# Kernel tuning notes

Hardware: AMD Instinct MI355X
Metric: run time of the kernel (lower is better)

## Reference

```python
import jax, jax.numpy as jnp
import numpy as np

T, B, I, H = 512, 256, 256, 256


def setup_inputs() -> dict:
    key = jax.random.key(0)
    ks = jax.random.split(key, 4)
    s = 1.0 / np.sqrt(I + H)  # fan-in scaling like nn.Linear default
    return {
        "x": jax.random.normal(ks[0], (T, B, I), dtype=jnp.float32),
        "h": jnp.zeros((B, H), dtype=jnp.float32),
        "Wz_w": jax.random.normal(ks[1], (H, I + H), dtype=jnp.float32) * s,
        "Wz_b": jnp.zeros((H,), dtype=jnp.float32),
        "Wr_w": jax.random.normal(ks[2], (H, I + H), dtype=jnp.float32) * s,
        "Wr_b": jnp.zeros((H,), dtype=jnp.float32),
        "W_w": jax.random.normal(ks[3], (H, I + H), dtype=jnp.float32) * s,
        "W_b": jnp.zeros((H,), dtype=jnp.float32),
    }


def reference(x, h, Wz_w, Wz_b, Wr_w, Wr_b, W_w, W_b):
    # x: [T, B, I], h: [B, H]. Gate input order is cat(h, x) as in the torch code.
    def step(h, xt):
        gate = jnp.concatenate([h, xt], axis=1)              # [B, H+I]
        zt = jax.nn.sigmoid(gate @ Wz_w.T + Wz_b)            # [B, H]
        rt = jax.nn.sigmoid(gate @ Wr_w.T + Wr_b)            # [B, H]
        cand_in = jnp.concatenate([rt * h, xt], axis=1)      # [B, H+I]
        ht = (1.0 - zt) * h + zt * jnp.tanh(cand_in @ W_w.T + W_b)
        return ht, ht

    h_final, hAll = jax.lax.scan(step, h, x)                 # hAll: [T, B, H]
    return hAll, h_final
```

## Files before the change

### kernel.cpp

```cpp
#include <hip/hip_runtime.h>


typedef float f32x4 __attribute__((ext_vector_type(4)));
typedef short bf16x8 __attribute__((ext_vector_type(8)));

__device__ __forceinline__ unsigned short f2bf(float f) {
  union { float f; unsigned int u; } v; v.f = f;
  unsigned int u = v.u + 0x7fffu + ((v.u >> 16) & 1u);
  return (unsigned short)(u >> 16);
}
__device__ __forceinline__ float u2f(unsigned int u) {
  union { unsigned int u; float f; } v; v.u = u; return v.f;
}
__device__ __forceinline__ unsigned int cvt_pk_bf16(float lo, float hi) {
  unsigned int r;
  asm("v_cvt_pk_bf16_f32 %0, %1, %2" : "=v"(r) : "v"(lo), "v"(hi));
  return r;
}
__device__ __forceinline__ float sigmoid_f(float x) {
  return __builtin_amdgcn_rcpf(1.f + __expf(-x));
}
__device__ __forceinline__ float tanh_f(float x) {
  float e = __expf(2.f * x);
  return 1.f - 2.f * __builtin_amdgcn_rcpf(e + 1.f);
}
__device__ __forceinline__ f32x4 unpk(uint2 gv) {
  f32x4 a;
  a[0] = u2f(gv.x << 16); a[1] = u2f(gv.x & 0xffff0000u);
  a[2] = u2f(gv.y << 16); a[3] = u2f(gv.y & 0xffff0000u);
  return a;
}
__device__ __forceinline__ int frag_off(int j, int b) {
  return ((j >> 5) * 64 + ((j >> 3) & 3) * 16 + b) * 8 + (j & 7);
}

__global__ __launch_bounds__(256) void gru_gx_kernel(
    const float* __restrict__ x,
    const float* __restrict__ Wz, const float* __restrict__ Wr, const float* __restrict__ Wc,
    const float* __restrict__ bz, const float* __restrict__ br, const float* __restrict__ bc,
    unsigned short* __restrict__ gx)
{
  __shared__ __align__(16) unsigned short As[64][72];
  __shared__ __align__(16) unsigned short Bs[256][72];

  const int tid  = threadIdx.x;
  const int lane = tid & 63;
  const int wid  = tid >> 6;
  const int l15  = lane & 15;
  const int lg   = lane >> 4;
  const int m0   = blockIdx.x * 64;
  const int gate = blockIdx.y;
  const float* W    = (gate == 0) ? Wz : ((gate == 1) ? Wr : Wc);
  const float* bias = (gate == 0) ? bz : ((gate == 1) ? br : bc);

  f32x4 acc[16];
  #pragma unroll
  for (int n = 0; n < 16; ++n) acc[n] = (f32x4){0.f, 0.f, 0.f, 0.f};

  for (int k0 = 0; k0 < 256; k0 += 64) {
    #pragma unroll
    for (int i = 0; i < 4; ++i) {
      int idx = tid + i * 256;
      int row = idx >> 4;
      int kq  = (idx & 15) << 2;
      float4 v = *(const float4*)(x + (size_t)(m0 + row) * 256 + k0 + kq);
      uint2 p; p.x = cvt_pk_bf16(v.x, v.y); p.y = cvt_pk_bf16(v.z, v.w);
      *(uint2*)&As[row][kq] = p;
    }
    #pragma unroll
    for (int i = 0; i < 16; ++i) {
      int idx = tid + i * 256;
      int row = idx >> 4;
      int kq  = (idx & 15) << 2;
      float4 v = *(const float4*)(W + (size_t)row * 512 + 256 + k0 + kq);
      uint2 p; p.x = cvt_pk_bf16(v.x, v.y); p.y = cvt_pk_bf16(v.z, v.w);
      *(uint2*)&Bs[row][kq] = p;
    }
    __syncthreads();
    #pragma unroll
    for (int ks = 0; ks < 64; ks += 32) {
      bf16x8 af = *(const bf16x8*)&As[wid * 16 + l15][ks + lg * 8];
      #pragma unroll
      for (int n = 0; n < 16; ++n) {
        bf16x8 bf = *(const bf16x8*)&Bs[n * 16 + l15][ks + lg * 8];
        acc[n] = __builtin_amdgcn_mfma_f32_16x16x32_bf16(af, bf, acc[n], 0, 0, 0);
      }
    }
    __syncthreads();
  }

  unsigned short* Ts = &Bs[0][0];
  const int TS = 268;
  #pragma unroll
  for (int n = 0; n < 16; ++n) {
    const int j = n * 16 + l15;
    float bv = bias[j];
    #pragma unroll
    for (int r = 0; r < 4; ++r) {
      unsigned int pk = cvt_pk_bf16(acc[n][r] + bv, 0.f);
      Ts[(wid * 16 + lg * 4 + r) * TS + j] = (unsigned short)pk;
    }
  }
  __syncthreads();

  const int tt  = m0 >> 8;
  const int bg0 = (m0 & 255) >> 4;
  #pragma unroll
  for (int i = 0; i < 8; ++i) {
    int idx  = tid + i * 256;
    int bg_l = idx >> 9;
    int rem  = idx & 511;
    int cb_l = rem >> 3;
    int bp   = rem & 7;
    int m    = bg_l * 16 + bp * 2;
    uint2 lo = *(const uint2*)&Ts[(size_t)m * TS + cb_l * 4];
    uint2 hi = *(const uint2*)&Ts[(size_t)(m + 1) * TS + cb_l * 4];
    uint4 val; val.x = lo.x; val.y = lo.y; val.z = hi.x; val.w = hi.y;
    size_t off = (((size_t)tt * 16 + bg0 + bg_l) * 192 + gate * 64 + cb_l) * 64
                 + (size_t)bp * 8;
    *(uint4*)(gx + off) = val;
  }
}

__global__ __launch_bounds__(512, 1) void gru_rec_kernel(
    const unsigned short* __restrict__ gx,
    const float* __restrict__ h0,
    const float* __restrict__ Wz, const float* __restrict__ Wr, const float* __restrict__ Wc,
    float* __restrict__ out)
{
  __shared__ __align__(16) unsigned short hA[4096];
  __shared__ __align__(16) unsigned short rhA[4096];

  const int tid   = threadIdx.x;
  const int lane  = tid & 63;
  const int wid   = tid >> 6;
  const int l15   = lane & 15;
  const int lg    = lane >> 4;
  const int wg    = blockIdx.x;
  const int brow0 = wg * 16;
  const int cb    = wid * 32;

  bf16x8 wz[2][8], wr[2][8], wc[2][8];
  #pragma unroll
  for (int n = 0; n < 2; ++n) {
    const int j = cb + n * 16 + l15;
    #pragma unroll
    for (int kk = 0; kk < 8; ++kk) {
      const int k = kk * 32 + lg * 8;
      #pragma unroll
      for (int g = 0; g < 3; ++g) {
        const float* W = (g == 0) ? Wz : ((g == 1) ? Wr : Wc);
        const float* p = W + (size_t)j * 512 + k;
        float4 a = *(const float4*)p;
        float4 b = *(const float4*)(p + 4);
        bf16x8 f;
        f[0] = (short)f2bf(a.x); f[1] = (short)f2bf(a.y);
        f[2] = (short)f2bf(a.z); f[3] = (short)f2bf(a.w);
        f[4] = (short)f2bf(b.x); f[5] = (short)f2bf(b.y);
        f[6] = (short)f2bf(b.z); f[7] = (short)f2bf(b.w);
        if (g == 0) wz[n][kk] = f; else if (g == 1) wr[n][kk] = f; else wc[n][kk] = f;
      }
    }
  }

  f32x4 hreg[2];
  #pragma unroll
  for (int n = 0; n < 2; ++n)
    hreg[n] = *(const f32x4*)(h0 + (size_t)(brow0 + l15) * 256 + cb + n * 16 + lg * 4);
  for (int idx = tid; idx < 16 * 256; idx += 512) {
    int r = idx >> 8, c = idx & 255;
    hA[frag_off(c, r)] = f2bf(h0[(size_t)(brow0 + r) * 256 + c]);
  }

  uint2 g1z[2], g1r[2], g2[2];
  {
    const size_t tb = (size_t)wg * 12288;
    #pragma unroll
    for (int n = 0; n < 2; ++n) {
      g1z[n] = *(const uint2*)(gx + tb + (size_t)(wid * 8 + n * 4 + lg) * 64 + l15 * 4);
      g1r[n] = *(const uint2*)(gx + tb + (size_t)(64 + wid * 8 + n * 4 + lg) * 64 + l15 * 4);
      g2[n]  = *(const uint2*)(gx + tb + (size_t)(128 + wid * 8 + n * 4 + lg) * 64 + l15 * 4);
    }
  }
  __syncthreads();

  for (int t = 0; t < 512; ++t) {
    const int tn = (t < 511) ? (t + 1) : 511;
    const size_t tbn = ((size_t)tn * 16 + wg) * 12288;

    f32x4 accZ[2], accR[2];
    #pragma unroll
    for (int n = 0; n < 2; ++n) { accZ[n] = unpk(g1z[n]); accR[n] = unpk(g1r[n]); }
    #pragma unroll
    for (int n = 0; n < 2; ++n) {
      g1z[n] = *(const uint2*)(gx + tbn + (size_t)(wid * 8 + n * 4 + lg) * 64 + l15 * 4);
      g1r[n] = *(const uint2*)(gx + tbn + (size_t)(64 + wid * 8 + n * 4 + lg) * 64 + l15 * 4);
    }

    #pragma unroll
    for (int kk = 0; kk < 8; ++kk) {
      bf16x8 hf = *(const bf16x8*)&hA[kk * 512 + lane * 8];
      accZ[0] = __builtin_amdgcn_mfma_f32_16x16x32_bf16(wz[0][kk], hf, accZ[0], 0, 0, 0);
      accZ[1] = __builtin_amdgcn_mfma_f32_16x16x32_bf16(wz[1][kk], hf, accZ[1], 0, 0, 0);
      accR[0] = __builtin_amdgcn_mfma_f32_16x16x32_bf16(wr[0][kk], hf, accR[0], 0, 0, 0);
      accR[1] = __builtin_amdgcn_mfma_f32_16x16x32_bf16(wr[1][kk], hf, accR[1], 0, 0, 0);
    }
    f32x4 zreg[2];
    #pragma unroll
    for (int n = 0; n < 2; ++n) {
      #pragma unroll
      for (int r = 0; r < 4; ++r) zreg[n][r] = sigmoid_f(accZ[n][r]);
      float rh0 = sigmoid_f(accR[n][0]) * hreg[n][0];
      float rh1 = sigmoid_f(accR[n][1]) * hreg[n][1];
      float rh2 = sigmoid_f(accR[n][2]) * hreg[n][2];
      float rh3 = sigmoid_f(accR[n][3]) * hreg[n][3];
      uint2 pk; pk.x = cvt_pk_bf16(rh0, rh1); pk.y = cvt_pk_bf16(rh2, rh3);
      *(uint2*)&rhA[frag_off(cb + n * 16 + lg * 4, l15)] = pk;
    }
    asm volatile("s_waitcnt lgkmcnt(0)" ::: "memory");
    __builtin_amdgcn_s_barrier();
    __builtin_amdgcn_sched_barrier(0);

    f32x4 acc2[2];
    #pragma unroll
    for (int n = 0; n < 2; ++n) acc2[n] = unpk(g2[n]);
    #pragma unroll
    for (int n = 0; n < 2; ++n)
      g2[n] = *(const uint2*)(gx + tbn + (size_t)(128 + wid * 8 + n * 4 + lg) * 64 + l15 * 4);

    #pragma unroll
    for (int kk = 0; kk < 8; ++kk) {
      bf16x8 rf = *(const bf16x8*)&rhA[kk * 512 + lane * 8];
      acc2[0] = __builtin_amdgcn_mfma_f32_16x16x32_bf16(wc[0][kk], rf, acc2[0], 0, 0, 0);
      acc2[1] = __builtin_amdgcn_mfma_f32_16x16x32_bf16(wc[1][kk], rf, acc2[1], 0, 0, 0);
    }
    #pragma unroll
    for (int n = 0; n < 2; ++n) {
      #pragma unroll
      for (int r = 0; r < 4; ++r) {
        float th = tanh_f(acc2[n][r]);
        hreg[n][r] = hreg[n][r] + zreg[n][r] * (th - hreg[n][r]);
      }
      *(f32x4*)(out + (size_t)t * 65536 + (size_t)(brow0 + l15) * 256 + cb + n * 16 + lg * 4) = hreg[n];
      if (t == 511)
        *(f32x4*)(out + (size_t)33554432 + (size_t)(brow0 + l15) * 256 + cb + n * 16 + lg * 4) = hreg[n];
      uint2 pk; pk.x = cvt_pk_bf16(hreg[n][0], hreg[n][1]);
      pk.y = cvt_pk_bf16(hreg[n][2], hreg[n][3]);
      *(uint2*)&hA[frag_off(cb + n * 16 + lg * 4, l15)] = pk;
    }
    asm volatile("s_waitcnt lgkmcnt(0)" ::: "memory");
    __builtin_amdgcn_s_barrier();
    __builtin_amdgcn_sched_barrier(0);
  }
}

extern "C" void kernel_launch(void* const* d_in, const int* in_sizes, int n_in,
                              void* d_out, int out_size, void* d_ws, size_t ws_size,
                              hipStream_t stream) {
  const float* x  = (const float*)d_in[0];
  const float* h0 = (const float*)d_in[1];
  const float* Wz = (const float*)d_in[2];
  const float* bz = (const float*)d_in[3];
  const float* Wr = (const float*)d_in[4];
  const float* br = (const float*)d_in[5];
  const float* Wc = (const float*)d_in[6];
  const float* bc = (const float*)d_in[7];
  float* out = (float*)d_out;
  unsigned short* gxbuf = (unsigned short*)d_ws;

  dim3 gridA(2048, 3);
  gru_gx_kernel<<<gridA, 256, 0, stream>>>(x, Wz, Wr, Wc, bz, br, bc, gxbuf);
  gru_rec_kernel<<<16, 512, 0, stream>>>(gxbuf, h0, Wz, Wr, Wc, out);
}
```

Before: 1.042 ms.

## Fuse input-projection GEMM and recurrence into one kernel with per-timestep flags

Merges the gate-input GEMM and the sequential recurrence into one launch. The first 16 blocks run the recurrence, and the remaining blocks compute the gx tiles, each bumping a per-timestep atomic counter when its tile is written. Recurrence blocks spin on these counters so they can start before all of gx exists, overlapping the bulk GEMM with the serial loop. The risks are deadlock if the producer blocks never get scheduled (a spin budget limits the wait), plus extra memset and polling overhead. The GEMM blocks now run at 512 threads with half of them idle, which lowers the GEMM's efficiency.

```diff
diff --git a/kernel.cpp b/kernel.cpp
--- a/kernel.cpp
+++ b/kernel.cpp
@@ -3,6 +3,9 @@
 
 typedef float f32x4 __attribute__((ext_vector_type(4)));
 typedef short bf16x8 __attribute__((ext_vector_type(8)));
+
+#define GX_SHORTS 100663296
+#define GX_BYTES  201326592
 
 __device__ __forceinline__ unsigned short f2bf(float f) {
   union { float f; unsigned int u; } v; v.f = f;
@@ -34,56 +37,83 @@
   return ((j >> 5) * 64 + ((j >> 3) & 3) * 16 + b) * 8 + (j & 7);
 }
 
-__global__ __launch_bounds__(256) void gru_gx_kernel(
+__device__ __forceinline__ int extend_ready(const int* done, int ready, int target) {
+  int budget = 1 << 24;
+  while (ready < target && budget-- > 0) {
+    int v[8];
+    #pragma unroll
+    for (int i = 0; i < 8; ++i) {
+      int idx = ready + 1 + i; if (idx > 511) idx = 511;
+      v[i] = __hip_atomic_load(&done[idx], __ATOMIC_RELAXED, __HIP_MEMORY_SCOPE_AGENT);
+    }
+    int k = 0;
+    #pragma unroll
+    for (int i = 0; i < 8; ++i) if (i == k && v[i] >= 12) k = i + 1;
+    if (k > 0) {
+      ready += k; if (ready > 511) ready = 511;
+      __threadfence();
+    }
+  }
+  return ready;
+}
+
+__device__ void a_role(
+    int lin, int tid,
     const float* __restrict__ x,
     const float* __restrict__ Wz, const float* __restrict__ Wr, const float* __restrict__ Wc,
     const float* __restrict__ bz, const float* __restrict__ br, const float* __restrict__ bc,
-    unsigned short* __restrict__ gx)
+    unsigned short* __restrict__ gx, int* done)
 {
   __shared__ __align__(16) unsigned short As[64][72];
   __shared__ __align__(16) unsigned short Bs[256][72];
 
-  const int tid  = threadIdx.x;
+  const int t    = lin / 12;
+  const int sub  = lin % 12;
+  const int gate = sub >> 2;
+  const int m0   = t * 256 + (sub & 3) * 64;
+  const float* W    = (gate == 0) ? Wz : ((gate == 1) ? Wr : Wc);
+  const float* bias = (gate == 0) ? bz : ((gate == 1) ? br : bc);
+
   const int lane = tid & 63;
   const int wid  = tid >> 6;
   const int l15  = lane & 15;
   const int lg   = lane >> 4;
-  const int m0   = blockIdx.x * 64;
-  const int gate = blockIdx.y;
-  const float* W    = (gate == 0) ? Wz : ((gate == 1) ? Wr : Wc);
-  const float* bias = (gate == 0) ? bz : ((gate == 1) ? br : bc);
 
   f32x4 acc[16];
   #pragma unroll
   for (int n = 0; n < 16; ++n) acc[n] = (f32x4){0.f, 0.f, 0.f, 0.f};
 
   for (int k0 = 0; k0 < 256; k0 += 64) {
-    #pragma unroll
-    for (int i = 0; i < 4; ++i) {
-      int idx = tid + i * 256;
-      int row = idx >> 4;
-      int kq  = (idx & 15) << 2;
-      float4 v = *(const float4*)(x + (size_t)(m0 + row) * 256 + k0 + kq);
-      uint2 p; p.x = cvt_pk_bf16(v.x, v.y); p.y = cvt_pk_bf16(v.z, v.w);
-      *(uint2*)&As[row][kq] = p;
-    }
-    #pragma unroll
-    for (int i = 0; i < 16; ++i) {
-      int idx = tid + i * 256;
-      int row = idx >> 4;
-      int kq  = (idx & 15) << 2;
-      float4 v = *(const float4*)(W + (size_t)row * 512 + 256 + k0 + kq);
-      uint2 p; p.x = cvt_pk_bf16(v.x, v.y); p.y = cvt_pk_bf16(v.z, v.w);
-      *(uint2*)&Bs[row][kq] = p;
+    if (tid < 256) {
+      #pragma unroll
+      for (int i = 0; i < 4; ++i) {
+        int idx = tid + i * 256;
+        int row = idx >> 4;
+        int kq  = (idx & 15) << 2;
+        float4 v = *(const float4*)(x + (size_t)(m0 + row) * 256 + k0 + kq);
+        uint2 p; p.x = cvt_pk_bf16(v.x, v.y); p.y = cvt_pk_bf16(v.z, v.w);
+        *(uint2*)&As[row][kq] = p;
+      }
+      #pragma unroll
+      for (int i = 0; i < 16; ++i) {
+        int idx = tid + i * 256;
+        int row = idx >> 4;
+        int kq  = (idx & 15) << 2;
+        float4 v = *(const float4*)(W + (size_t)row * 512 + 256 + k0 + kq);
+        uint2 p; p.x = cvt_pk_bf16(v.x, v.y); p.y = cvt_pk_bf16(v.z, v.w);
+        *(uint2*)&Bs[row][kq] = p;
+      }
     }
     __syncthreads();
-    #pragma unroll
-    for (int ks = 0; ks < 64; ks += 32) {
-      bf16x8 af = *(const bf16x8*)&As[wid * 16 + l15][ks + lg * 8];
-      #pragma unroll
-      for (int n = 0; n < 16; ++n) {
-        bf16x8 bf = *(const bf16x8*)&Bs[n * 16 + l15][ks + lg * 8];
-        acc[n] = __builtin_amdgcn_mfma_f32_16x16x32_bf16(af, bf, acc[n], 0, 0, 0);
+    if (tid < 256) {
+      #pragma unroll
+      for (int ks = 0; ks < 64; ks += 32) {
+        bf16x8 af = *(const bf16x8*)&As[wid * 16 + l15][ks + lg * 8];
+        #pragma unroll
+        for (int n = 0; n < 16; ++n) {
+          bf16x8 bf = *(const bf16x8*)&Bs[n * 16 + l15][ks + lg * 8];
+          acc[n] = __builtin_amdgcn_mfma_f32_16x16x32_bf16(af, bf, acc[n], 0, 0, 0);
+        }
       }
     }
     __syncthreads();
@@ -91,52 +121,57 @@
 
   unsigned short* Ts = &Bs[0][0];
   const int TS = 268;
-  #pragma unroll
-  for (int n = 0; n < 16; ++n) {
-    const int j = n * 16 + l15;
-    float bv = bias[j];
-    #pragma unroll
-    for (int r = 0; r < 4; ++r) {
-      unsigned int pk = cvt_pk_bf16(acc[n][r] + bv, 0.f);
-      Ts[(wid * 16 + lg * 4 + r) * TS + j] = (unsigned short)pk;
+  if (tid < 256) {
+    #pragma unroll
+    for (int n = 0; n < 16; ++n) {
+      const int j = n * 16 + l15;
+      float bv = bias[j];
+      #pragma unroll
+      for (int r = 0; r < 4; ++r) {
+        unsigned int pk = cvt_pk_bf16(acc[n][r] + bv, 0.f);
+        Ts[(wid * 16 + lg * 4 + r) * TS + j] = (unsigned short)pk;
+      }
     }
   }
   __syncthreads();
 
-  const int tt  = m0 >> 8;
   const int bg0 = (m0 & 255) >> 4;
-  #pragma unroll
-  for (int i = 0; i < 8; ++i) {
-    int idx  = tid + i * 256;
-    int bg_l = idx >> 9;
-    int rem  = idx & 511;
-    int cb_l = rem >> 3;
-    int bp   = rem & 7;
-    int m    = bg_l * 16 + bp * 2;
-    uint2 lo = *(const uint2*)&Ts[(size_t)m * TS + cb_l * 4];
-    uint2 hi = *(const uint2*)&Ts[(size_t)(m + 1) * TS + cb_l * 4];
-    uint4 val; val.x = lo.x; val.y = lo.y; val.z = hi.x; val.w = hi.y;
-    size_t off = (((size_t)tt * 16 + bg0 + bg_l) * 192 + gate * 64 + cb_l) * 64
-                 + (size_t)bp * 8;
-    *(uint4*)(gx + off) = val;
-  }
-}
-
-__global__ __launch_bounds__(512, 1) void gru_rec_kernel(
+  if (tid < 256) {
+    #pragma unroll
+    for (int i = 0; i < 8; ++i) {
+      int idx  = tid + i * 256;
+      int bg_l = idx >> 9;
+      int rem  = idx & 511;
+      int cb_l = rem >> 3;
+      int bp   = rem & 7;
+      int m    = bg_l * 16 + bp * 2;
+      uint2 lo = *(const uint2*)&Ts[(size_t)m * TS + cb_l * 4];
+      uint2 hi = *(const uint2*)&Ts[(size_t)(m + 1) * TS + cb_l * 4];
+      uint4 val; val.x = lo.x; val.y = lo.y; val.z = hi.x; val.w = hi.y;
+      size_t off = (((size_t)t * 16 + bg0 + bg_l) * 192 + gate * 64 + cb_l) * 64
+                   + (size_t)bp * 8;
+      *(uint4*)(gx + off) = val;
+    }
+  }
+  __syncthreads();
+  if (done && tid == 0)
+    __hip_atomic_fetch_add(&done[t], 1, __ATOMIC_RELEASE, __HIP_MEMORY_SCOPE_AGENT);
+}
+
+__device__ void b_role(
+    int wg, int tid,
     const unsigned short* __restrict__ gx,
     const float* __restrict__ h0,
     const float* __restrict__ Wz, const float* __restrict__ Wr, const float* __restrict__ Wc,
-    float* __restrict__ out)
+    float* __restrict__ out, const int* done)
 {
   __shared__ __align__(16) unsigned short hA[4096];
   __shared__ __align__(16) unsigned short rhA[4096];
 
-  const int tid   = threadIdx.x;
   const int lane  = tid & 63;
   const int wid   = tid >> 6;
   const int l15   = lane & 15;
   const int lg    = lane >> 4;
-  const int wg    = blockIdx.x;
   const int brow0 = wg * 16;
   const int cb    = wid * 32;
 
@@ -172,6 +207,9 @@
     hA[frag_off(c, r)] = f2bf(h0[(size_t)(brow0 + r) * 256 + c]);
   }
 
+  int ready = -1;
+  if (done) ready = extend_ready(done, ready, 0);
+
   uint2 g1z[2], g1r[2], g2[2];
   {
     const size_t tb = (size_t)wg * 12288;
@@ -187,6 +225,8 @@
   for (int t = 0; t < 512; ++t) {
     const int tn = (t < 511) ? (t + 1) : 511;
     const size_t tbn = ((size_t)tn * 16 + wg) * 12288;
+
+    if (done) ready = extend_ready(done, ready, tn);
 
     f32x4 accZ[2], accR[2];
     #pragma unroll
@@ -252,6 +292,36 @@
     __builtin_amdgcn_s_barrier();
     __builtin_amdgcn_sched_barrier(0);
   }
+}
+
+__global__ __launch_bounds__(512, 1) void gru_fused_kernel(
+    const float* __restrict__ x, const float* __restrict__ h0,
+    const float* __restrict__ Wz, const float* __restrict__ Wr, const float* __restrict__ Wc,
+    const float* __restrict__ bz, const float* __restrict__ br, const float* __restrict__ bc,
+    unsigned short* __restrict__ gx, float* __restrict__ out, int* done)
+{
+  if (blockIdx.x < 16)
+    b_role(blockIdx.x, threadIdx.x, gx, h0, Wz, Wr, Wc, out, done);
+  else
+    a_role(blockIdx.x - 16, threadIdx.x, x, Wz, Wr, Wc, bz, br, bc, gx, done);
+}
+
+__global__ __launch_bounds__(512, 1) void gru_gx_kernel(
+    const float* __restrict__ x,
+    const float* __restrict__ Wz, const float* __restrict__ Wr, const float* __restrict__ Wc,
+    const float* __restrict__ bz, const float* __restrict__ br, const float* __restrict__ bc,
+    unsigned short* __restrict__ gx)
+{
+  a_role(blockIdx.x, threadIdx.x, x, Wz, Wr, Wc, bz, br, bc, gx, nullptr);
+}
+
+__global__ __launch_bounds__(512, 1) void gru_rec_kernel(
+    const unsigned short* __restrict__ gx,
+    const float* __restrict__ h0,
+    const float* __restrict__ Wz, const float* __restrict__ Wr, const float* __restrict__ Wc,
+    float* __restrict__ out)
+{
+  b_role(blockIdx.x, threadIdx.x, gx, h0, Wz, Wr, Wc, out, nullptr);
 }
 
 extern "C" void kernel_launch(void* const* d_in, const int* in_sizes, int n_in,
@@ -268,7 +338,13 @@
   float* out = (float*)d_out;
   unsigned short* gxbuf = (unsigned short*)d_ws;
 
-  dim3 gridA(2048, 3);
-  gru_gx_kernel<<<gridA, 256, 0, stream>>>(x, Wz, Wr, Wc, bz, br, bc, gxbuf);
-  gru_rec_kernel<<<16, 512, 0, stream>>>(gxbuf, h0, Wz, Wr, Wc, out);
-}
+  if (ws_size >= (size_t)GX_BYTES + 4096) {
+    int* done = (int*)((char*)d_ws + GX_BYTES);
+    hipMemsetAsync(done, 0, 2048, stream);
+    gru_fused_kernel<<<6160, 512, 0, stream>>>(x, h0, Wz, Wr, Wc, bz, br, bc,
+                                               gxbuf, out, done);
+  } else {
+    gru_gx_kernel<<<6144, 512, 0, stream>>>(x, Wz, Wr, Wc, bz, br, bc, gxbuf);
+    gru_rec_kernel<<<16, 512, 0, stream>>>(gxbuf, h0, Wz, Wr, Wc, out);
+  }
+}
```

Result: slower. 1.967 ms (+88.8%).
